# Optimization experiments

Measured on AMD Instinct MI355X. Metric: run time of the kernel, lower is better.

## Reference

```python
import jax, jax.numpy as jnp
import numpy as np

N = 50000
E = 800000
IN_C = 64
OUT_C = 128
T = 4


def setup_inputs() -> dict:
    key = jax.random.key(0)
    ks = jax.random.split(key, 12)
    s = 0.05
    return {
        "x": jax.random.normal(ks[0], (N, IN_C), dtype=jnp.float32),
        "u": jax.random.normal(ks[1], (N, OUT_C), dtype=jnp.float32),
        "edge_index": jax.random.randint(ks[2], (2, E), 0, N, dtype=jnp.int32),
        # w1: Linear(in_channels, out_channels)
        "w1_W": jax.random.normal(ks[3], (OUT_C, IN_C), dtype=jnp.float32) * s,
        "w1_b": jnp.zeros((OUT_C,), dtype=jnp.float32),
        # sigmod MLP: three Linear(out, out) layers
        "m1_W": jax.random.normal(ks[4], (OUT_C, OUT_C), dtype=jnp.float32) * s,
        "m1_b": jnp.zeros((OUT_C,), dtype=jnp.float32),
        "m2_W": jax.random.normal(ks[5], (OUT_C, OUT_C), dtype=jnp.float32) * s,
        "m2_b": jnp.zeros((OUT_C,), dtype=jnp.float32),
        "m3_W": jax.random.normal(ks[6], (OUT_C, OUT_C), dtype=jnp.float32) * s,
        "m3_b": jnp.zeros((OUT_C,), dtype=jnp.float32),
        # w2: Linear(out, out) for graph readout
        "w2_W": jax.random.normal(ks[7], (OUT_C, OUT_C), dtype=jnp.float32) * s,
        "w2_b": jnp.zeros((OUT_C,), dtype=jnp.float32),
    }


def reference(x, u, edge_index, w1_W, w1_b, m1_W, m1_b, m2_W, m2_b, m3_W, m3_b, w2_W, w2_b):
    n_nodes = x.shape[0]
    src = edge_index[0]  # gather source (u_j)
    dst = edge_index[1]  # scatter-add target
    xw = x @ w1_W.T + w1_b  # [N, out]; identical every iteration
    for _ in range(T):
        agg = jax.ops.segment_sum(u[src], dst, num_segments=n_nodes)  # [N, out]
        h = jax.nn.relu(agg @ m1_W.T + m1_b)
        h = jax.nn.relu(h @ m2_W.T + m2_b)
        h = jnp.tanh(h @ m3_W.T + m3_b)
        u = jax.nn.relu(xw + h)
    g = jnp.sum(u, axis=0, keepdims=True)  # e @ u with e = ones [1, N]
    return g @ w2_W.T + w2_b  # [1, out]
```

## Files before the change

### kernel.cpp

```cpp
#include <hip/hip_runtime.h>
#include <hip/hip_bf16.h>

#define NN 50000
#define NE 800000
#define CI 64
#define CO 128
#define SCANB 49
#define NB 196
#define CHUNK 2048
#define NCH 391

typedef __attribute__((ext_vector_type(8))) short bf16x8;
typedef __attribute__((ext_vector_type(4))) float f32x4;

__device__ __forceinline__ unsigned short f2bf(float f) {
  unsigned int u = __float_as_uint(f);
  u += 0x7fffu + ((u >> 16) & 1u);
  return (unsigned short)(u >> 16);
}
__device__ __forceinline__ float bf2f_lo(unsigned int p) { return __uint_as_float(p << 16); }
__device__ __forceinline__ float bf2f_hi(unsigned int p) { return __uint_as_float(p & 0xffff0000u); }
__device__ __forceinline__ unsigned int pk2(float lo, float hi) {
  return ((unsigned int)f2bf(hi) << 16) | (unsigned int)f2bf(lo);
}


__global__ __launch_bounds__(256) void k_bhist(const int* __restrict__ dst,
                                               int* __restrict__ bcnt) {
  __shared__ int lc[NB];
  int tid = threadIdx.x;
  for (int t = tid; t < NB; t += 256) lc[t] = 0;
  __syncthreads();
  int base = blockIdx.x * CHUNK;
#pragma unroll
  for (int i = 0; i < 8; ++i) {
    int idx = base + i * 256 + tid;
    if (idx < NE) atomicAdd(&lc[dst[idx] >> 8], 1);
  }
  __syncthreads();
  for (int t = tid; t < NB; t += 256) if (lc[t]) atomicAdd(&bcnt[t], lc[t]);
}

__global__ __launch_bounds__(256) void k_bscan(const int* __restrict__ bcnt,
                                               int* __restrict__ bkt_off,
                                               int* __restrict__ bkt_cur) {
  __shared__ int s[256];
  int t = threadIdx.x;
  int v = (t < NB) ? bcnt[t] : 0;
  s[t] = v;
  __syncthreads();
  for (int off = 1; off < 256; off <<= 1) {
    int x = (t >= off) ? s[t - off] : 0;
    __syncthreads();
    s[t] += x;
    __syncthreads();
  }
  if (t < NB) { int e = s[t] - v; bkt_off[t] = e; bkt_cur[t] = e; }
  if (t == 0) bkt_off[NB] = NE;
}

__global__ __launch_bounds__(256) void k_bin(const int* __restrict__ src,
                                             const int* __restrict__ dst,
                                             int* __restrict__ bkt_cur,
                                             uint2* __restrict__ pairs) {
  __shared__ int lcnt[NB];
  __shared__ int lbase[NB];
  int tid = threadIdx.x;
  for (int t = tid; t < NB; t += 256) lcnt[t] = 0;
  __syncthreads();
  int base = blockIdx.x * CHUNK;
  int ds[8], sr[8], rk[8];
#pragma unroll
  for (int i = 0; i < 8; ++i) {
    int idx = base + i * 256 + tid;
    if (idx < NE) {
      ds[i] = dst[idx]; sr[i] = src[idx];
      rk[i] = atomicAdd(&lcnt[ds[i] >> 8], 1);
    } else ds[i] = -1;
  }
  __syncthreads();
  for (int t = tid; t < NB; t += 256)
    lbase[t] = lcnt[t] ? atomicAdd(&bkt_cur[t], lcnt[t]) : 0;
  __syncthreads();
#pragma unroll
  for (int i = 0; i < 8; ++i) {
    if (ds[i] >= 0) {
      uint2 pr; pr.x = (unsigned)sr[i]; pr.y = (unsigned)ds[i];
      pairs[lbase[ds[i] >> 8] + rk[i]] = pr;
    }
  }
}

__global__ __launch_bounds__(256) void k_deg(const uint2* __restrict__ pairs,
                                             const int* __restrict__ bkt_off,
                                             int* __restrict__ deg) {
  __shared__ int lc[256];
  int t = threadIdx.x, b = blockIdx.x;
  lc[t] = 0;
  __syncthreads();
  int beg = bkt_off[b], end = bkt_off[b + 1];
  for (int i = beg + t; i < end; i += 256)
    atomicAdd(&lc[pairs[i].y & 255], 1);
  __syncthreads();
  int node = (b << 8) + t;
  if (node < NN) deg[node] = lc[t];
}

__global__ __launch_bounds__(256) void k_scan1(const int* __restrict__ deg, int* __restrict__ bsum) {
  int i0 = blockIdx.x * 1024 + threadIdx.x * 4;
  int s = 0;
#pragma unroll
  for (int j = 0; j < 4; ++j) { int i = i0 + j; if (i < NN) s += deg[i]; }
#pragma unroll
  for (int off = 32; off; off >>= 1) s += __shfl_down(s, off);
  __shared__ int ws[4];
  if ((threadIdx.x & 63) == 0) ws[threadIdx.x >> 6] = s;
  __syncthreads();
  if (threadIdx.x == 0) bsum[blockIdx.x] = ws[0] + ws[1] + ws[2] + ws[3];
}

__global__ __launch_bounds__(64) void k_scan2(const int* __restrict__ bsum, int* __restrict__ boff) {
  int t = threadIdx.x;
  int v = (t < SCANB) ? bsum[t] : 0;
  int incl = v;
#pragma unroll
  for (int off = 1; off < 64; off <<= 1) {
    int o = __shfl_up(incl, off);
    if (t >= off) incl += o;
  }
  if (t < SCANB) boff[t] = incl - v;
}

__global__ __launch_bounds__(256) void k_scan3(const int* __restrict__ deg, const int* __restrict__ boff,
                                               int* __restrict__ row_off) {
  int b = blockIdx.x;
  int i0 = b * 1024 + threadIdx.x * 4;
  int v[4]; int tsum = 0;
#pragma unroll
  for (int j = 0; j < 4; ++j) { int i = i0 + j; v[j] = (i < NN) ? deg[i] : 0; tsum += v[j]; }
  int incl = tsum;
#pragma unroll
  for (int off = 1; off < 64; off <<= 1) {
    int o = __shfl_up(incl, off);
    if ((threadIdx.x & 63) >= (unsigned)off) incl += o;
  }
  __shared__ int ws[4];
  int w = threadIdx.x >> 6;
  if ((threadIdx.x & 63) == 63) ws[w] = incl;
  __syncthreads();
  int wbase = 0;
  for (int k = 0; k < 4; ++k) if (k < w) wbase += ws[k];
  int excl = boff[b] + wbase + incl - tsum;
#pragma unroll
  for (int j = 0; j < 4; ++j) { int i = i0 + j; if (i < NN) row_off[i] = excl; excl += v[j]; }
  if (b == 0 && threadIdx.x == 0) row_off[NN] = NE;
}

__global__ __launch_bounds__(256) void k_fillB(const uint2* __restrict__ pairs,
                                               const int* __restrict__ bkt_off,
                                               const int* __restrict__ row_off,
                                               int* __restrict__ ssrc) {
  __shared__ int lcur[256];
  int t = threadIdx.x, b = blockIdx.x;
  lcur[t] = 0;
  __syncthreads();
  int beg = bkt_off[b], end = bkt_off[b + 1];
  for (int i = beg + t; i < end; i += 256) {
    uint2 e = pairs[i];
    int d = (int)e.y;
    int pos = row_off[d] + atomicAdd(&lcur[d & 255], 1);
    ssrc[pos] = (int)e.x;
  }
}

__global__ void k_cvt_w(const float* __restrict__ w1, const float* __restrict__ m1,
                        const float* __restrict__ m2, const float* __restrict__ m3,
                        unsigned short* __restrict__ o) {
  int i = blockIdx.x * blockDim.x + threadIdx.x;
  if (i >= 57344) return;
  float v;
  if (i < 8192) v = w1[i];
  else if (i < 24576) v = m1[i - 8192];
  else if (i < 40960) v = m2[i - 24576];
  else v = m3[i - 40960];
  o[i] = f2bf(v);
}

__global__ void k_cvt4(const float* __restrict__ in, unsigned short* __restrict__ out, int n4) {
  int i = blockIdx.x * blockDim.x + threadIdx.x;
  if (i >= n4) return;
  float4 v = *(const float4*)(in + i * 4);
  ushort2 lo = { f2bf(v.x), f2bf(v.y) };
  ushort2 hi = { f2bf(v.z), f2bf(v.w) };
  *(ushort2*)(out + i * 4) = lo;
  *(ushort2*)(out + i * 4 + 2) = hi;
}

__global__ __launch_bounds__(256) void k_gather(const int* __restrict__ row_off,
    const int* __restrict__ ssrc, const unsigned short* __restrict__ ubf,
    unsigned short* __restrict__ agg) {
  int node = blockIdx.x * 4 + (threadIdx.x >> 6);
  if (node >= NN) return;
  int lane = threadIdx.x & 63;
  int eg = lane >> 4, c = lane & 15;
  int beg = row_off[node], end = row_off[node + 1];
  float a[8];
#pragma unroll
  for (int i = 0; i < 8; ++i) a[i] = 0.f;

#define ADD8(r) { a[0] += bf2f_lo(r.x); a[1] += bf2f_hi(r.x); \
                  a[2] += bf2f_lo(r.y); a[3] += bf2f_hi(r.y); \
                  a[4] += bf2f_lo(r.z); a[5] += bf2f_hi(r.z); \
                  a[6] += bf2f_lo(r.w); a[7] += bf2f_hi(r.w); }

  for (int base = beg; base < end; base += 64) {
    int e = base + lane;
    int sid = (e < end) ? ssrc[e] : 0;
    int cnt = min(64, end - base);
    int j = 0;
    for (; j + 16 <= cnt; j += 16) {
      int s0 = __shfl(sid, j + 0 + eg);
      int s1 = __shfl(sid, j + 4 + eg);
      int s2 = __shfl(sid, j + 8 + eg);
      int s3 = __shfl(sid, j + 12 + eg);
      uint4 r0 = *(const uint4*)(ubf + (size_t)s0 * CO + c * 8);
      uint4 r1 = *(const uint4*)(ubf + (size_t)s1 * CO + c * 8);
      uint4 r2 = *(const uint4*)(ubf + (size_t)s2 * CO + c * 8);
      uint4 r3 = *(const uint4*)(ubf + (size_t)s3 * CO + c * 8);
      ADD8(r0); ADD8(r1); ADD8(r2); ADD8(r3);
    }
    for (; j + 4 <= cnt; j += 4) {
      int s = __shfl(sid, j + eg);
      uint4 r = *(const uint4*)(ubf + (size_t)s * CO + c * 8);
      ADD8(r);
    }
    if (j < cnt) {
      int rem = cnt - j;
      int s = __shfl(sid, j + min(eg, rem - 1));
      if (eg < rem) {
        uint4 r = *(const uint4*)(ubf + (size_t)s * CO + c * 8);
        ADD8(r);
      }
    }
  }
#undef ADD8
#pragma unroll
  for (int i = 0; i < 8; ++i) { a[i] += __shfl_xor(a[i], 16); a[i] += __shfl_xor(a[i], 32); }
  if (lane < 16) {
    uint4 o;
    o.x = pk2(a[0], a[1]); o.y = pk2(a[2], a[3]);
    o.z = pk2(a[4], a[5]); o.w = pk2(a[6], a[7]);
    *(uint4*)(agg + (size_t)node * CO + c * 8) = o;
  }
}

__global__ __launch_bounds__(256) void k_xw(const unsigned short* __restrict__ A,
    const unsigned short* __restrict__ W, const float* __restrict__ bias,
    unsigned short* __restrict__ xwb) {
  int wave = threadIdx.x >> 6, lane = threadIdx.x & 63;
  int m = lane & 15, q = lane >> 4;
  int row0 = blockIdx.x * 64 + wave * 16;
  int arow = row0 + m; if (arow >= NN) arow = NN - 1;
  const unsigned short* Ar = A + (size_t)arow * CI;
  f32x4 acc[8];
#pragma unroll
  for (int tt = 0; tt < 8; ++tt) acc[tt] = (f32x4){0.f, 0.f, 0.f, 0.f};
#pragma unroll
  for (int ks = 0; ks < CI; ks += 32) {
    bf16x8 a = *(const bf16x8*)(Ar + ks + q * 8);
#pragma unroll
    for (int tt = 0; tt < 8; ++tt) {
      bf16x8 b = *(const bf16x8*)(W + (size_t)(tt * 16 + m) * CI + ks + q * 8);
      acc[tt] = __builtin_amdgcn_mfma_f32_16x16x32_bf16(a, b, acc[tt], 0, 0, 0);
    }
  }
#pragma unroll
  for (int tt = 0; tt < 8; ++tt) {
    int o = tt * 16 + m;
    float bv = bias[o];
#pragma unroll
    for (int r = 0; r < 4; ++r) {
      int node = row0 + q * 4 + r;
      if (node < NN) xwb[(size_t)node * CO + o] = f2bf(acc[tt][r] + bv);
    }
  }
}

__global__ __launch_bounds__(512, 4) void k_mlp(const unsigned short* __restrict__ agg,
    const unsigned short* __restrict__ W1, const unsigned short* __restrict__ W2,
    const unsigned short* __restrict__ W3,
    const float* __restrict__ b1, const float* __restrict__ b2, const float* __restrict__ b3,
    const unsigned short* __restrict__ xwb, unsigned short* __restrict__ uout) {
  constexpr int SP = 136;
  __shared__ unsigned short lds[16384 + 8 * 16 * SP];
  unsigned short* wt = lds;
  int tid = threadIdx.x;
  int wave = tid >> 6, lane = tid & 63;
  int m = lane & 15, q = lane >> 4;
  int row0 = blockIdx.x * 128 + wave * 16;
  unsigned short* L = lds + 16384 + wave * 16 * SP;
  int ar = row0 + m; if (ar >= NN) ar = NN - 1;
  const unsigned short* Ap = agg + (size_t)ar * CO;

  uint4 wreg[4];
  const int trb = (tid >> 4) & 7;
  const int tc  = tid & 15;
  const int ldst0 = (tid >> 4) * 128 + ((tc ^ trb) << 3);
  auto stage_load = [&](const unsigned short* W) {
#pragma unroll
    for (int j = 0; j < 4; ++j)
      wreg[j] = *(const uint4*)(W + ((j * 512 + tid) << 3));
  };
  auto stage_write = [&]() {
#pragma unroll
    for (int j = 0; j < 4; ++j)
      *(uint4*)(wt + ldst0 + j * 4096) = wreg[j];
  };
  auto bfrag = [&](int t, int ks) -> bf16x8 {
    int ch = (ks >> 3) + q;
    return *(const bf16x8*)(wt + (t * 16 + m) * 128 + ((ch ^ (m & 7)) << 3));
  };

  stage_load(W1);
  bf16x8 ar4[4];
#pragma unroll
  for (int k4 = 0; k4 < 4; ++k4) ar4[k4] = *(const bf16x8*)(Ap + k4 * 32 + q * 8);
  stage_write();

  f32x4 acc[8];
#pragma unroll
  for (int t = 0; t < 8; ++t) acc[t] = (f32x4){0.f, 0.f, 0.f, 0.f};
  __syncthreads();

#pragma unroll
  for (int k4 = 0; k4 < 4; ++k4) {
#pragma unroll
    for (int t = 0; t < 8; ++t) {
      bf16x8 b = bfrag(t, k4 * 32);
      acc[t] = __builtin_amdgcn_mfma_f32_16x16x32_bf16(ar4[k4], b, acc[t], 0, 0, 0);
    }
  }
  stage_load(W2);
#pragma unroll
  for (int t = 0; t < 8; ++t) {
    float bv = b1[t * 16 + m];
#pragma unroll
    for (int r = 0; r < 4; ++r)
      L[(q * 4 + r) * SP + t * 16 + m] = f2bf(fmaxf(acc[t][r] + bv, 0.f));
  }
  __syncthreads();
  stage_write();
#pragma unroll
  for (int t = 0; t < 8; ++t) acc[t] = (f32x4){0.f, 0.f, 0.f, 0.f};
  __syncthreads();

#pragma unroll
  for (int ks = 0; ks < CO; ks += 32) {
    bf16x8 a = *(const bf16x8*)(L + m * SP + ks + q * 8);
#pragma unroll
    for (int t = 0; t < 8; ++t) {
      bf16x8 b = bfrag(t, ks);
      acc[t] = __builtin_amdgcn_mfma_f32_16x16x32_bf16(a, b, acc[t], 0, 0, 0);
    }
  }
  stage_load(W3);
#pragma unroll
  for (int t = 0; t < 8; ++t) {
    float bv = b2[t * 16 + m];
#pragma unroll
    for (int r = 0; r < 4; ++r)
      L[(q * 4 + r) * SP + t * 16 + m] = f2bf(fmaxf(acc[t][r] + bv, 0.f));
  }
  __syncthreads();
  stage_write();
#pragma unroll
  for (int t = 0; t < 8; ++t) acc[t] = (f32x4){0.f, 0.f, 0.f, 0.f};
  __syncthreads();

#pragma unroll
  for (int ks = 0; ks < CO; ks += 32) {
    bf16x8 a = *(const bf16x8*)(L + m * SP + ks + q * 8);
#pragma unroll
    for (int t = 0; t < 8; ++t) {
      bf16x8 b = bfrag(t, ks);
      acc[t] = __builtin_amdgcn_mfma_f32_16x16x32_bf16(a, b, acc[t], 0, 0, 0);
    }
  }
#pragma unroll
  for (int t = 0; t < 8; ++t) {
    float bv = b3[t * 16 + m];
#pragma unroll
    for (int r = 0; r < 4; ++r) {
      float v = acc[t][r] + bv;
      float e = __expf(2.f * v);
      v = 1.f - 2.f / (e + 1.f);
      L[(q * 4 + r) * SP + t * 16 + m] = f2bf(v);
    }
  }
  int ln = lane >> 2, lc = lane & 3;
  int gnode = row0 + ln;
  if (gnode < NN) {
    const unsigned short* xr = xwb + (size_t)gnode * CO;
    unsigned short* ur = uout + (size_t)gnode * CO;
#pragma unroll
    for (int rnd = 0; rnd < 4; ++rnd) {
      int ch = (rnd * 4 + lc) * 8;
      uint4 h = *(const uint4*)(L + ln * SP + ch);
      uint4 xv = *(const uint4*)(xr + ch);
      uint4 o;
      o.x = pk2(fmaxf(bf2f_lo(h.x) + bf2f_lo(xv.x), 0.f), fmaxf(bf2f_hi(h.x) + bf2f_hi(xv.x), 0.f));
      o.y = pk2(fmaxf(bf2f_lo(h.y) + bf2f_lo(xv.y), 0.f), fmaxf(bf2f_hi(h.y) + bf2f_hi(xv.y), 0.f));
      o.z = pk2(fmaxf(bf2f_lo(h.z) + bf2f_lo(xv.z), 0.f), fmaxf(bf2f_hi(h.z) + bf2f_hi(xv.z), 0.f));
      o.w = pk2(fmaxf(bf2f_lo(h.w) + bf2f_lo(xv.w), 0.f), fmaxf(bf2f_hi(h.w) + bf2f_hi(xv.w), 0.f));
      *(uint4*)(ur + ch) = o;
    }
  }
}

__global__ __launch_bounds__(256) void k_reduce(const unsigned short* __restrict__ u,
                                                float* __restrict__ g) {
  int ch2 = threadIdx.x & 63;
  int sub = threadIdx.x >> 6;
  float a0 = 0.f, a1 = 0.f;
  for (int n = blockIdx.x * 4 + sub; n < NN; n += gridDim.x * 4) {
    unsigned int p = *(const unsigned int*)(u + (size_t)n * CO + ch2 * 2);
    a0 += bf2f_lo(p); a1 += bf2f_hi(p);
  }
  __shared__ float s0[256], s1[256];
  s0[threadIdx.x] = a0; s1[threadIdx.x] = a1;
  __syncthreads();
  if (sub == 0) {
    a0 = s0[ch2] + s0[64 + ch2] + s0[128 + ch2] + s0[192 + ch2];
    a1 = s1[ch2] + s1[64 + ch2] + s1[128 + ch2] + s1[192 + ch2];
    atomicAdd(&g[ch2 * 2], a0);
    atomicAdd(&g[ch2 * 2 + 1], a1);
  }
}

__global__ void k_final(const float* __restrict__ g, const float* __restrict__ w2,
                        const float* __restrict__ b2, float* __restrict__ outp) {
  __shared__ float sg[128];
  if (threadIdx.x < 128) sg[threadIdx.x] = g[threadIdx.x];
  __syncthreads();
  int j = threadIdx.x;
  if (j < 128) {
    float acc = b2[j];
    for (int c = 0; c < 128; ++c) acc += sg[c] * w2[j * 128 + c];
    outp[j] = acc;
  }
}

extern "C" void kernel_launch(void* const* d_in, const int* in_sizes, int n_in,
                              void* d_out, int out_size, void* d_ws, size_t ws_size,
                              hipStream_t stream) {
  (void)in_sizes; (void)n_in; (void)out_size; (void)ws_size;
  const float* x   = (const float*)d_in[0];
  const float* u0  = (const float*)d_in[1];
  const int*   ei  = (const int*)d_in[2];
  const float* w1W = (const float*)d_in[3];
  const float* w1b = (const float*)d_in[4];
  const float* m1W = (const float*)d_in[5];
  const float* m1b = (const float*)d_in[6];
  const float* m2W = (const float*)d_in[7];
  const float* m2b = (const float*)d_in[8];
  const float* m3W = (const float*)d_in[9];
  const float* m3b = (const float*)d_in[10];
  const float* w2W = (const float*)d_in[11];
  const float* w2b = (const float*)d_in[12];
  const int* esrc = ei;
  const int* edst = ei + NE;

  char* p = (char*)d_ws;
  auto carve = [&](size_t bytes) { char* r = p; p += (bytes + 255) & ~(size_t)255; return r; };
  unsigned short* xwb     = (unsigned short*)carve((size_t)NN * CO * 2);
  unsigned short* ubf     = (unsigned short*)carve((size_t)NN * CO * 2);
  unsigned short* agg     = (unsigned short*)carve((size_t)NN * CO * 2);
  unsigned short* xb      = (unsigned short*)carve((size_t)NN * CI * 2);
  unsigned short* wbf     = (unsigned short*)carve((size_t)57344 * 2);
  int*            row_off = (int*)carve((size_t)(NN + 1) * 4);
  int*            deg     = (int*)carve((size_t)NN * 4);
  int*            ssrc    = (int*)carve((size_t)NE * 4);
  uint2*          pairs   = (uint2*)carve((size_t)NE * 8);
  int*            bkt_cnt = (int*)carve((size_t)NB * 4);
  int*            bkt_off = (int*)carve((size_t)(NB + 1) * 4);
  int*            bkt_cur = (int*)carve((size_t)NB * 4);
  int*            bsum    = (int*)carve((size_t)SCANB * 4);
  int*            boff    = (int*)carve((size_t)SCANB * 4);
  float*          g       = (float*)carve(128 * 4);

  hipMemsetAsync(bkt_cnt, 0, (size_t)NB * 4, stream);
  hipMemsetAsync(g, 0, 128 * 4, stream);

  k_bhist<<<NCH, 256, 0, stream>>>(edst, bkt_cnt);
  k_bscan<<<1, 256, 0, stream>>>(bkt_cnt, bkt_off, bkt_cur);
  k_bin<<<NCH, 256, 0, stream>>>(esrc, edst, bkt_cur, pairs);
  k_deg<<<NB, 256, 0, stream>>>(pairs, bkt_off, deg);
  k_scan1<<<SCANB, 256, 0, stream>>>(deg, bsum);
  k_scan2<<<1, 64, 0, stream>>>(bsum, boff);
  k_scan3<<<SCANB, 256, 0, stream>>>(deg, boff, row_off);
  k_fillB<<<NB, 256, 0, stream>>>(pairs, bkt_off, row_off, ssrc);

  k_cvt_w<<<(57344 + 255) / 256, 256, 0, stream>>>(w1W, m1W, m2W, m3W, wbf);
  k_cvt4<<<(NN * CI / 4 + 255) / 256, 256, 0, stream>>>(x, xb, NN * CI / 4);
  k_cvt4<<<(NN * CO / 4 + 255) / 256, 256, 0, stream>>>(u0, ubf, NN * CO / 4);

  k_xw<<<(NN + 63) / 64, 256, 0, stream>>>(xb, wbf, w1b, xwb);

  const unsigned short* Wm1 = wbf + 8192;
  const unsigned short* Wm2 = wbf + 8192 + 16384;
  const unsigned short* Wm3 = wbf + 8192 + 2 * 16384;
  const int GM = (NN + 127) / 128;
  for (int it = 0; it < 4; ++it) {
    k_gather<<<(NN + 3) / 4, 256, 0, stream>>>(row_off, ssrc, ubf, agg);
    k_mlp<<<GM, 512, 0, stream>>>(agg, Wm1, Wm2, Wm3, m1b, m2b, m3b, xwb, ubf);
  }

  k_reduce<<<256, 256, 0, stream>>>(ubf, g);
  k_final<<<1, 128, 0, stream>>>(g, w2W, w2b, (float*)d_out);
}
```

Baseline: 410.3 us.

## Fuse neighbor gather into MLP kernel with ping-pong u buffers

Removes the separate gather kernel. Each wave of the MLP kernel now aggregates its own 16 nodes' neighbor features into LDS, then runs the three-layer MLP reading A fragments from LDS. Two u buffers are swapped each iteration because the kernel now reads the old u while writing the new one. This drops the agg round trip through global memory and one launch per iteration. The cost is that the gather now runs on only 391 blocks with serial per-node loops per wave, which lowers the memory-level parallelism available for the random gathers.

After: 448.9 us. +9.4%, slower.

```diff
diff --git a/kernel.cpp b/kernel.cpp
--- a/kernel.cpp
+++ b/kernel.cpp
@@ -23,7 +23,6 @@
 __device__ __forceinline__ unsigned int pk2(float lo, float hi) {
   return ((unsigned int)f2bf(hi) << 16) | (unsigned int)f2bf(lo);
 }
-
 
 __global__ __launch_bounds__(256) void k_bhist(const int* __restrict__ dst,
                                                int* __restrict__ bcnt) {
@@ -196,64 +195,6 @@
   *(ushort2*)(out + i * 4 + 2) = hi;
 }
 
-__global__ __launch_bounds__(256) void k_gather(const int* __restrict__ row_off,
-    const int* __restrict__ ssrc, const unsigned short* __restrict__ ubf,
-    unsigned short* __restrict__ agg) {
-  int node = blockIdx.x * 4 + (threadIdx.x >> 6);
-  if (node >= NN) return;
-  int lane = threadIdx.x & 63;
-  int eg = lane >> 4, c = lane & 15;
-  int beg = row_off[node], end = row_off[node + 1];
-  float a[8];
-#pragma unroll
-  for (int i = 0; i < 8; ++i) a[i] = 0.f;
-
-#define ADD8(r) { a[0] += bf2f_lo(r.x); a[1] += bf2f_hi(r.x); \
-                  a[2] += bf2f_lo(r.y); a[3] += bf2f_hi(r.y); \
-                  a[4] += bf2f_lo(r.z); a[5] += bf2f_hi(r.z); \
-                  a[6] += bf2f_lo(r.w); a[7] += bf2f_hi(r.w); }
-
-  for (int base = beg; base < end; base += 64) {
-    int e = base + lane;
-    int sid = (e < end) ? ssrc[e] : 0;
-    int cnt = min(64, end - base);
-    int j = 0;
-    for (; j + 16 <= cnt; j += 16) {
-      int s0 = __shfl(sid, j + 0 + eg);
-      int s1 = __shfl(sid, j + 4 + eg);
-      int s2 = __shfl(sid, j + 8 + eg);
-      int s3 = __shfl(sid, j + 12 + eg);
-      uint4 r0 = *(const uint4*)(ubf + (size_t)s0 * CO + c * 8);
-      uint4 r1 = *(const uint4*)(ubf + (size_t)s1 * CO + c * 8);
-      uint4 r2 = *(const uint4*)(ubf + (size_t)s2 * CO + c * 8);
-      uint4 r3 = *(const uint4*)(ubf + (size_t)s3 * CO + c * 8);
-      ADD8(r0); ADD8(r1); ADD8(r2); ADD8(r3);
-    }
-    for (; j + 4 <= cnt; j += 4) {
-      int s = __shfl(sid, j + eg);
-      uint4 r = *(const uint4*)(ubf + (size_t)s * CO + c * 8);
-      ADD8(r);
-    }
-    if (j < cnt) {
-      int rem = cnt - j;
-      int s = __shfl(sid, j + min(eg, rem - 1));
-      if (eg < rem) {
-        uint4 r = *(const uint4*)(ubf + (size_t)s * CO + c * 8);
-        ADD8(r);
-      }
-    }
-  }
-#undef ADD8
-#pragma unroll
-  for (int i = 0; i < 8; ++i) { a[i] += __shfl_xor(a[i], 16); a[i] += __shfl_xor(a[i], 32); }
-  if (lane < 16) {
-    uint4 o;
-    o.x = pk2(a[0], a[1]); o.y = pk2(a[2], a[3]);
-    o.z = pk2(a[4], a[5]); o.w = pk2(a[6], a[7]);
-    *(uint4*)(agg + (size_t)node * CO + c * 8) = o;
-  }
-}
-
 __global__ __launch_bounds__(256) void k_xw(const unsigned short* __restrict__ A,
     const unsigned short* __restrict__ W, const float* __restrict__ bias,
     unsigned short* __restrict__ xwb) {
@@ -286,11 +227,13 @@
   }
 }
 
-__global__ __launch_bounds__(512, 4) void k_mlp(const unsigned short* __restrict__ agg,
+__global__ __launch_bounds__(512, 4) void k_fused(
+    const unsigned short* __restrict__ ucur,
+    const int* __restrict__ row_off, const int* __restrict__ ssrc,
     const unsigned short* __restrict__ W1, const unsigned short* __restrict__ W2,
     const unsigned short* __restrict__ W3,
     const float* __restrict__ b1, const float* __restrict__ b2, const float* __restrict__ b3,
-    const unsigned short* __restrict__ xwb, unsigned short* __restrict__ uout) {
+    const unsigned short* __restrict__ xwb, unsigned short* __restrict__ unxt) {
   constexpr int SP = 136;
   __shared__ unsigned short lds[16384 + 8 * 16 * SP];
   unsigned short* wt = lds;
@@ -299,8 +242,60 @@
   int m = lane & 15, q = lane >> 4;
   int row0 = blockIdx.x * 128 + wave * 16;
   unsigned short* L = lds + 16384 + wave * 16 * SP;
-  int ar = row0 + m; if (ar >= NN) ar = NN - 1;
-  const unsigned short* Ap = agg + (size_t)ar * CO;
+  int eg = lane >> 4, c = lane & 15;
+
+#define ADD8(r) { a[0] += bf2f_lo(r.x); a[1] += bf2f_hi(r.x); \
+                  a[2] += bf2f_lo(r.y); a[3] += bf2f_hi(r.y); \
+                  a[4] += bf2f_lo(r.z); a[5] += bf2f_hi(r.z); \
+                  a[6] += bf2f_lo(r.w); a[7] += bf2f_hi(r.w); }
+  for (int n16 = 0; n16 < 16; ++n16) {
+    int node = row0 + n16;
+    float a[8];
+#pragma unroll
+    for (int i = 0; i < 8; ++i) a[i] = 0.f;
+    if (node < NN) {
+      int beg = row_off[node], end = row_off[node + 1];
+      for (int base = beg; base < end; base += 64) {
+        int e = base + lane;
+        int sid = (e < end) ? ssrc[e] : 0;
+        int cnt = min(64, end - base);
+        int j = 0;
+        for (; j + 16 <= cnt; j += 16) {
+          int s0 = __shfl(sid, j + 0 + eg);
+          int s1 = __shfl(sid, j + 4 + eg);
+          int s2 = __shfl(sid, j + 8 + eg);
+          int s3 = __shfl(sid, j + 12 + eg);
+          uint4 r0 = *(const uint4*)(ucur + (size_t)s0 * CO + c * 8);
+          uint4 r1 = *(const uint4*)(ucur + (size_t)s1 * CO + c * 8);
+          uint4 r2 = *(const uint4*)(ucur + (size_t)s2 * CO + c * 8);
+          uint4 r3 = *(const uint4*)(ucur + (size_t)s3 * CO + c * 8);
+          ADD8(r0); ADD8(r1); ADD8(r2); ADD8(r3);
+        }
+        for (; j + 4 <= cnt; j += 4) {
+          int s = __shfl(sid, j + eg);
+          uint4 r = *(const uint4*)(ucur + (size_t)s * CO + c * 8);
+          ADD8(r);
+        }
+        if (j < cnt) {
+          int rem = cnt - j;
+          int s = __shfl(sid, j + min(eg, rem - 1));
+          if (eg < rem) {
+            uint4 r = *(const uint4*)(ucur + (size_t)s * CO + c * 8);
+            ADD8(r);
+          }
+        }
+      }
+#pragma unroll
+      for (int i = 0; i < 8; ++i) { a[i] += __shfl_xor(a[i], 16); a[i] += __shfl_xor(a[i], 32); }
+    }
+    if (lane < 16) {
+      uint4 o;
+      o.x = pk2(a[0], a[1]); o.y = pk2(a[2], a[3]);
+      o.z = pk2(a[4], a[5]); o.w = pk2(a[6], a[7]);
+      *(uint4*)(L + n16 * SP + c * 8) = o;
+    }
+  }
+#undef ADD8
 
   uint4 wreg[4];
   const int trb = (tid >> 4) & 7;
@@ -322,22 +317,19 @@
   };
 
   stage_load(W1);
-  bf16x8 ar4[4];
-#pragma unroll
-  for (int k4 = 0; k4 < 4; ++k4) ar4[k4] = *(const bf16x8*)(Ap + k4 * 32 + q * 8);
   stage_write();
-
   f32x4 acc[8];
 #pragma unroll
   for (int t = 0; t < 8; ++t) acc[t] = (f32x4){0.f, 0.f, 0.f, 0.f};
   __syncthreads();
 
 #pragma unroll
-  for (int k4 = 0; k4 < 4; ++k4) {
+  for (int ks = 0; ks < CO; ks += 32) {
+    bf16x8 a = *(const bf16x8*)(L + m * SP + ks + q * 8);
 #pragma unroll
     for (int t = 0; t < 8; ++t) {
-      bf16x8 b = bfrag(t, k4 * 32);
-      acc[t] = __builtin_amdgcn_mfma_f32_16x16x32_bf16(ar4[k4], b, acc[t], 0, 0, 0);
+      bf16x8 b = bfrag(t, ks);
+      acc[t] = __builtin_amdgcn_mfma_f32_16x16x32_bf16(a, b, acc[t], 0, 0, 0);
     }
   }
   stage_load(W2);
@@ -401,7 +393,7 @@
   int gnode = row0 + ln;
   if (gnode < NN) {
     const unsigned short* xr = xwb + (size_t)gnode * CO;
-    unsigned short* ur = uout + (size_t)gnode * CO;
+    unsigned short* ur = unxt + (size_t)gnode * CO;
 #pragma unroll
     for (int rnd = 0; rnd < 4; ++rnd) {
       int ch = (rnd * 4 + lc) * 8;
@@ -474,7 +466,7 @@
   auto carve = [&](size_t bytes) { char* r = p; p += (bytes + 255) & ~(size_t)255; return r; };
   unsigned short* xwb     = (unsigned short*)carve((size_t)NN * CO * 2);
   unsigned short* ubf     = (unsigned short*)carve((size_t)NN * CO * 2);
-  unsigned short* agg     = (unsigned short*)carve((size_t)NN * CO * 2);
+  unsigned short* upp     = (unsigned short*)carve((size_t)NN * CO * 2);
   unsigned short* xb      = (unsigned short*)carve((size_t)NN * CI * 2);
   unsigned short* wbf     = (unsigned short*)carve((size_t)57344 * 2);
   int*            row_off = (int*)carve((size_t)(NN + 1) * 4);
@@ -510,11 +502,14 @@
   const unsigned short* Wm2 = wbf + 8192 + 16384;
   const unsigned short* Wm3 = wbf + 8192 + 2 * 16384;
   const int GM = (NN + 127) / 128;
+  const unsigned short* uc = ubf;
+  unsigned short* un = upp;
   for (int it = 0; it < 4; ++it) {
-    k_gather<<<(NN + 3) / 4, 256, 0, stream>>>(row_off, ssrc, ubf, agg);
-    k_mlp<<<GM, 512, 0, stream>>>(agg, Wm1, Wm2, Wm3, m1b, m2b, m3b, xwb, ubf);
-  }
-
-  k_reduce<<<256, 256, 0, stream>>>(ubf, g);
+    k_fused<<<GM, 512, 0, stream>>>(uc, row_off, ssrc, Wm1, Wm2, Wm3,
+                                    m1b, m2b, m3b, xwb, un);
+    const unsigned short* t = uc; uc = un; un = (unsigned short*)t;
+  }
+
+  k_reduce<<<256, 256, 0, stream>>>(uc, g);
   k_final<<<1, 128, 0, stream>>>(g, w2W, w2b, (float*)d_out);
 }
```

## Map one 16-lane group per node in gather, four nodes per wave

Applied to the files above, without the earlier changes.

The gather kernel now gives each node a 16-lane quarter-wave instead of a full 64-lane wave. Each group loads up to 16 edge sources and walks them sequentially, which removes the cross-group shuffle-xor reduction and lets one wave handle four nodes. This cuts idle lanes for low-degree nodes (average degree is about 16). Groups in the same wave now diverge when their degrees differ, and the grid is NN/16, which relies on NN being divisible by 16 with no bounds check.

New measurement: 412.9 us. About the same (+0.7%).

```diff
diff --git a/kernel.cpp b/kernel.cpp
--- a/kernel.cpp
+++ b/kernel.cpp
@@ -23,7 +23,6 @@
 __device__ __forceinline__ unsigned int pk2(float lo, float hi) {
   return ((unsigned int)f2bf(hi) << 16) | (unsigned int)f2bf(lo);
 }
-
 
 __global__ __launch_bounds__(256) void k_bhist(const int* __restrict__ dst,
                                                int* __restrict__ bcnt) {
@@ -199,10 +198,10 @@
 __global__ __launch_bounds__(256) void k_gather(const int* __restrict__ row_off,
     const int* __restrict__ ssrc, const unsigned short* __restrict__ ubf,
     unsigned short* __restrict__ agg) {
-  int node = blockIdx.x * 4 + (threadIdx.x >> 6);
-  if (node >= NN) return;
-  int lane = threadIdx.x & 63;
-  int eg = lane >> 4, c = lane & 15;
+  int wave = threadIdx.x >> 6, lane = threadIdx.x & 63;
+  int g = lane >> 4, c = lane & 15;
+  int node = blockIdx.x * 16 + wave * 4 + g;
+  int gl = g << 4;
   int beg = row_off[node], end = row_off[node + 1];
   float a[8];
 #pragma unroll
@@ -213,45 +212,33 @@
                   a[4] += bf2f_lo(r.z); a[5] += bf2f_hi(r.z); \
                   a[6] += bf2f_lo(r.w); a[7] += bf2f_hi(r.w); }
 
-  for (int base = beg; base < end; base += 64) {
-    int e = base + lane;
+  for (int base = beg; base < end; base += 16) {
+    int e = base + c;
     int sid = (e < end) ? ssrc[e] : 0;
-    int cnt = min(64, end - base);
+    int cnt = min(16, end - base);
     int j = 0;
-    for (; j + 16 <= cnt; j += 16) {
-      int s0 = __shfl(sid, j + 0 + eg);
-      int s1 = __shfl(sid, j + 4 + eg);
-      int s2 = __shfl(sid, j + 8 + eg);
-      int s3 = __shfl(sid, j + 12 + eg);
+    for (; j + 4 <= cnt; j += 4) {
+      int s0 = __shfl(sid, gl + j + 0);
+      int s1 = __shfl(sid, gl + j + 1);
+      int s2 = __shfl(sid, gl + j + 2);
+      int s3 = __shfl(sid, gl + j + 3);
       uint4 r0 = *(const uint4*)(ubf + (size_t)s0 * CO + c * 8);
       uint4 r1 = *(const uint4*)(ubf + (size_t)s1 * CO + c * 8);
       uint4 r2 = *(const uint4*)(ubf + (size_t)s2 * CO + c * 8);
       uint4 r3 = *(const uint4*)(ubf + (size_t)s3 * CO + c * 8);
       ADD8(r0); ADD8(r1); ADD8(r2); ADD8(r3);
     }
-    for (; j + 4 <= cnt; j += 4) {
-      int s = __shfl(sid, j + eg);
+    for (; j < cnt; ++j) {
+      int s = __shfl(sid, gl + j);
       uint4 r = *(const uint4*)(ubf + (size_t)s * CO + c * 8);
       ADD8(r);
     }
-    if (j < cnt) {
-      int rem = cnt - j;
-      int s = __shfl(sid, j + min(eg, rem - 1));
-      if (eg < rem) {
-        uint4 r = *(const uint4*)(ubf + (size_t)s * CO + c * 8);
-        ADD8(r);
-      }
-    }
   }
 #undef ADD8
-#pragma unroll
-  for (int i = 0; i < 8; ++i) { a[i] += __shfl_xor(a[i], 16); a[i] += __shfl_xor(a[i], 32); }
-  if (lane < 16) {
-    uint4 o;
-    o.x = pk2(a[0], a[1]); o.y = pk2(a[2], a[3]);
-    o.z = pk2(a[4], a[5]); o.w = pk2(a[6], a[7]);
-    *(uint4*)(agg + (size_t)node * CO + c * 8) = o;
-  }
+  uint4 o;
+  o.x = pk2(a[0], a[1]); o.y = pk2(a[2], a[3]);
+  o.z = pk2(a[4], a[5]); o.w = pk2(a[6], a[7]);
+  *(uint4*)(agg + (size_t)node * CO + c * 8) = o;
 }
 
 __global__ __launch_bounds__(256) void k_xw(const unsigned short* __restrict__ A,
@@ -511,7 +498,7 @@
   const unsigned short* Wm3 = wbf + 8192 + 2 * 16384;
   const int GM = (NN + 127) / 128;
   for (int it = 0; it < 4; ++it) {
-    k_gather<<<(NN + 3) / 4, 256, 0, stream>>>(row_off, ssrc, ubf, agg);
+    k_gather<<<NN / 16, 256, 0, stream>>>(row_off, ssrc, ubf, agg);
     k_mlp<<<GM, 512, 0, stream>>>(agg, Wm1, Wm2, Wm3, m1b, m2b, m3b, xwb, ubf);
   }
 
```
